# Kernel tuning notes

Measured on AMD Instinct MI355X. Metric: run time of the kernel, lower is better.

The kernel has to match this reference:

```python
import jax, jax.numpy as jnp
import numpy as np

WIN = 4          # ka_win_num (2x2 grid of windows)
KS = 3           # kernel_size
HEADS = 8
PAD = 1


def setup_inputs() -> dict:
    key = jax.random.key(0)
    ks = jax.random.split(key, 11)
    B, res, C = 8, 256, 64
    c16 = C // 16  # SE bottleneck (dim >= 64 branch)
    inp = {
        "x": jax.random.normal(ks[0], (B, res * res, C), dtype=jnp.float32),
        # per-window grouped-conv weights (the "kernels" fed to attention)
        "conv_w": jax.random.normal(ks[1], (WIN, C, C, KS, KS), dtype=jnp.float32) * 0.05,
        "qkv_w": jax.random.normal(ks[2], (C, 3 * C), dtype=jnp.float32) * 0.05,
        "qkv_b": jax.random.normal(ks[3], (3 * C,), dtype=jnp.float32) * 0.01,
        "proj_w": jax.random.normal(ks[4], (C, C), dtype=jnp.float32) * 0.05,
        "proj_b": jax.random.normal(ks[5], (C,), dtype=jnp.float32) * 0.01,
        # per-window SE params (1x1 convs on pooled (k,k))
        "se_w1": jax.random.normal(ks[6], (WIN, c16, C), dtype=jnp.float32) * 0.1,
        "se_b1": jax.random.normal(ks[7], (WIN, c16), dtype=jnp.float32) * 0.01,
        "se_w2": jax.random.normal(ks[8], (WIN, C, c16), dtype=jnp.float32) * 0.1,
        "se_b2": jax.random.normal(ks[9], (WIN, C), dtype=jnp.float32) * 0.01,
    }
    return inp


def reference(x, conv_w, qkv_w, qkv_b, proj_w, proj_b, se_w1, se_b1, se_w2, se_b2):
    B, L, C = x.shape
    H = int(round(np.sqrt(L)))
    g = int(round(np.sqrt(WIN)))      # windows per side = 2
    ws = H // g                       # window_size
    hd = C // HEADS
    scale = hd ** (-0.5)
    S = WIN * KS * KS                 # attention sequence length

    xw = x.reshape(B, g, ws, g, ws, C).transpose(1, 3, 0, 5, 2, 4)
    xw = xw.reshape(WIN, B, C, ws, ws)

    # ---- gather conv kernels as tokens: weight.view(out,in,k2).permute(0,2,1), concat over windows
    kern_tok = conv_w.reshape(WIN, C, C, KS * KS).transpose(1, 0, 3, 2).reshape(C, S, C)

    # ---- self-attention over kernel tokens (batch = C_out = dim)
    qkv = kern_tok @ qkv_w + qkv_b                                    # (C, S, 3C)
    qkv = qkv.reshape(C, S, 3, HEADS, hd).transpose(2, 0, 3, 1, 4)     # (3, C, H, S, hd)
    q, kk, v = qkv[0] * scale, qkv[1], qkv[2]
    attn = jax.nn.softmax(jnp.einsum('chsd,chtd->chst', q, kk), axis=-1)
    out = jnp.einsum('chst,chtd->chsd', attn, v)                       # (C, H, S, hd)
    out = out.transpose(0, 2, 1, 3).reshape(C, S, C)
    out = out @ proj_w + proj_b

    kern = out.reshape(C, WIN, KS, KS, C).transpose(1, 0, 4, 2, 3)

    # ---- SE over each window's kernel, treating (C_out, C_in, k, k) as (N, Ch, H, W)
    pool = kern.mean(axis=(-2, -1))
    h = jax.nn.relu(jnp.einsum('wnc,wdc->wnd', pool, se_w1) + se_b1[:, None, :])
    s = jax.nn.sigmoid(jnp.einsum('wnd,wcd->wnc', h, se_w2) + se_b2[:, None, :])
    kern = kern * s[..., None, None]

    def conv(xi, wi):
        return jax.lax.conv_general_dilated(xi, wi, (1, 1), [(PAD, PAD), (PAD, PAD)])

    y = jax.vmap(conv)(xw, kern)

    y = y.reshape(g, g, B, C, ws, ws).transpose(2, 0, 4, 1, 5, 3).reshape(B, H * H, C)
    return y
```

## Files before the change

kernel.cpp:

```cpp
#include <hip/hip_runtime.h>
#include <hip/hip_bf16.h>

typedef __bf16 bf16x8 __attribute__((ext_vector_type(8)));
typedef float  f32x4  __attribute__((ext_vector_type(4)));

__global__ __launch_bounds__(192) void qkv_kernel(
    const float* __restrict__ conv_w, const float* __restrict__ qkv_w,
    const float* __restrict__ qkv_b,
    float* __restrict__ qv, float* __restrict__ kvv, float* __restrict__ vv)
{
    __shared__ float tok[64];
    const int bid = blockIdx.x;
    const int co = bid / 36, s = bid - co * 36;
    const int w = s / 9, p = s - w * 9;
    const int t = threadIdx.x;
    if (t < 64) tok[t] = conv_w[(((w * 64 + co) * 64 + t) * 9) + p];
    __syncthreads();
    float acc = qkv_b[t];
#pragma unroll 8
    for (int ci = 0; ci < 64; ++ci) acc += tok[ci] * qkv_w[ci * 192 + t];
    const int trip = t >> 6, rem = t & 63, h = rem >> 3, d = rem & 7;
    if (trip == 0) acc *= 0.35355339059327373f;
    float* dst = (trip == 0) ? qv : ((trip == 1) ? kvv : vv);
    dst[((co * 8 + h) * 36 + s) * 8 + d] = acc;
}

__global__ __launch_bounds__(64) void attn_kernel(
    const float* __restrict__ qv, const float* __restrict__ kvv,
    const float* __restrict__ vv, float* __restrict__ ao)
{
    __shared__ float kl[288], vl[288];
    const int bid = blockIdx.x;
    const int t = threadIdx.x;
    const float* kb = kvv + bid * 288;
    const float* vb = vv + bid * 288;
    for (int i = t; i < 288; i += 64) { kl[i] = kb[i]; vl[i] = vb[i]; }
    __syncthreads();
    if (t < 36) {
        float q[8];
        const float* qb = qv + bid * 288 + t * 8;
#pragma unroll
        for (int d = 0; d < 8; ++d) q[d] = qb[d];
        float sc[36];
        float mx = -1e30f;
#pragma unroll
        for (int u = 0; u < 36; ++u) {
            float a = 0.f;
#pragma unroll
            for (int d = 0; d < 8; ++d) a += q[d] * kl[u * 8 + d];
            sc[u] = a;
            mx = fmaxf(mx, a);
        }
        float sum = 0.f;
        float o[8] = {0.f,0.f,0.f,0.f,0.f,0.f,0.f,0.f};
#pragma unroll
        for (int u = 0; u < 36; ++u) {
            float e = expf(sc[u] - mx);
            sum += e;
#pragma unroll
            for (int d = 0; d < 8; ++d) o[d] += e * vl[u * 8 + d];
        }
        const float inv = 1.0f / sum;
        const int co = bid >> 3, h = bid & 7;
        float* dst = ao + (co * 36 + t) * 64 + h * 8;
#pragma unroll
        for (int d = 0; d < 8; ++d) dst[d] = o[d] * inv;
    }
}

__global__ __launch_bounds__(64) void proj_se_kernel(
    const float* __restrict__ ao, const float* __restrict__ proj_w,
    const float* __restrict__ proj_b,
    const float* __restrict__ se_w1, const float* __restrict__ se_b1,
    const float* __restrict__ se_w2, const float* __restrict__ se_b2,
    ushort* __restrict__ kout)
{
    __shared__ float al[9][64];
    __shared__ float pool[64];
    __shared__ float hb[4];
    const int bid = blockIdx.x;
    const int w = bid >> 6, co = bid & 63;
    const int t = threadIdx.x;
    for (int i = t; i < 576; i += 64) {
        int p = i >> 6, j = i & 63;
        al[p][j] = ao[(co * 36 + w * 9 + p) * 64 + j];
    }
    __syncthreads();
    float kv[9];
#pragma unroll
    for (int p = 0; p < 9; ++p) {
        float a = proj_b[t];
#pragma unroll 8
        for (int j = 0; j < 64; ++j) a += al[p][j] * proj_w[j * 64 + t];
        kv[p] = a;
    }
    float pl = 0.f;
#pragma unroll
    for (int p = 0; p < 9; ++p) pl += kv[p];
    pool[t] = pl * (1.0f / 9.0f);
    __syncthreads();
    if (t < 4) {
        float hh = se_b1[w * 4 + t];
#pragma unroll 8
        for (int c = 0; c < 64; ++c) hh += pool[c] * se_w1[(w * 4 + t) * 64 + c];
        hb[t] = fmaxf(hh, 0.0f);
    }
    __syncthreads();
    float z = se_b2[w * 64 + t];
#pragma unroll
    for (int d = 0; d < 4; ++d) z += hb[d] * se_w2[(w * 64 + t) * 4 + d];
    const float sg = 1.0f / (1.0f + expf(-z));
    const int hhalf = t >> 5, ci32 = t & 31;
#pragma unroll
    for (int p = 0; p < 9; ++p) {
        __hip_bfloat16 hv = __float2bfloat16(kv[p] * sg);
        kout[(((hhalf * 4 + w) * 9) + p) * 2048 + co * 32 + ci32] = *(const ushort*)&hv;
    }
}

__global__ __launch_bounds__(256, 3) void conv_kernel(
    const float* __restrict__ x, const ushort* __restrict__ kern,
    float* __restrict__ out)
{
    __shared__ alignas(16) ushort in_lds[18 * 18 * 64];
    __shared__ alignas(16) ushort kn_lds[2 * 2048];

    const int tid = threadIdx.x;

    const int bid = blockIdx.x;
    const int nb  = ((bid & 7) << 8) + (bid >> 3);
    const int bz  = nb >> 6;
    const int rem = nb & 63;
    const int i0  = (rem >> 3) << 4;
    const int j0  = (rem & 7) << 4;
    const int w = bz >> 3, b = bz & 7;
    const int gi = w >> 1, gj = w & 1;

    const int wv   = tid >> 6;
    const int lane = tid & 63;
    const int l15  = lane & 15;
    const int hi4  = lane >> 4;

    const char* kern_b = (const char*)kern;
    const int ksrc = (lane << 4) ^ (((lane >> 3) & 3) << 4);
    auto stage_kern = [&](int s, int buf) {
        const int p = s >> 1, hh = s & 1;
        const char* gs = kern_b + ((size_t)((((hh * 4 + w) * 9)) + p) << 12);
        __builtin_amdgcn_global_load_lds(
            (const __attribute__((address_space(1))) unsigned int*)(gs + (wv << 10) + ksrc),
            (__attribute__((address_space(3))) unsigned int*)
                ((char*)kn_lds + (buf << 12) + (wv << 10)),
            16, 0, 0);
    };

    {
        const int cc = (tid & 15) << 2;
        const int p0 = tid >> 4;
#pragma unroll
        for (int half = 0; half < 2; ++half) {
            const int kbeg = half ? 11 : 0;
            const int kend = half ? 21 : 11;
            float4 v[11];
            unsigned okm = 0;
#pragma unroll
            for (int k = kbeg; k < kend; ++k) {
                const int pp = p0 + (k << 4);
                const int ppc = pp < 323 ? pp : 323;
                const int r = ppc / 18, q = ppc - r * 18;
                const int iy = i0 - 1 + r, jx = j0 - 1 + q;
                const bool ok = (pp < 324) & (iy >= 0) & (iy < 128) & (jx >= 0) & (jx < 128);
                const int iyc = iy < 0 ? 0 : (iy > 127 ? 127 : iy);
                const int jxc = jx < 0 ? 0 : (jx > 127 ? 127 : jx);
                const size_t xi = (((size_t)b << 16) +
                                   (size_t)(gi * 128 + iyc) * 256 + (size_t)(gj * 128 + jxc)) * 64 + cc;
                v[k - kbeg] = *(const float4*)(x + xi);
                okm |= (unsigned)ok << (k - kbeg);
            }
            if (half == 0) stage_kern(0, 0);
#pragma unroll
            for (int k = kbeg; k < kend; ++k) {
                const int pp = p0 + (k << 4);
                if (pp < 324) {
                    const int r = pp / 18, q = pp - r * 18;
                    float4 z = (okm >> (k - kbeg)) & 1 ? v[k - kbeg]
                                                       : make_float4(0.f, 0.f, 0.f, 0.f);
                    union { ushort4 u; ushort h4[4]; } tmp;
                    __hip_bfloat16 b0 = __float2bfloat16(z.x); tmp.h4[0] = *(const ushort*)&b0;
                    __hip_bfloat16 b1 = __float2bfloat16(z.y); tmp.h4[1] = *(const ushort*)&b1;
                    __hip_bfloat16 b2 = __float2bfloat16(z.z); tmp.h4[2] = *(const ushort*)&b2;
                    __hip_bfloat16 b3 = __float2bfloat16(z.w); tmp.h4[3] = *(const ushort*)&b3;
                    *(ushort4*)((char*)in_lds +
                        ((pp << 7) + ((cc << 1) ^ ((q & 7) << 4)))) = tmp.u;
                }
            }
        }
    }

    f32x4 acc[4][4];
#pragma unroll
    for (int mf = 0; mf < 4; ++mf)
#pragma unroll
        for (int nf = 0; nf < 4; ++nf)
            acc[mf][nf] = (f32x4){0.f, 0.f, 0.f, 0.f};

    __syncthreads();

#pragma unroll
    for (int s = 0; s < 18; ++s) {
        const int buf = s & 1;
        if (s < 17) stage_kern(s + 1, buf ^ 1);

        const int p = s >> 1, hh = s & 1;
        const int kh = p / 3, kw = p - kh * 3;

        bf16x8 Kf[4];
#pragma unroll
        for (int nf = 0; nf < 4; ++nf) {
            const int co = nf * 16 + l15;
            Kf[nf] = *(const bf16x8*)((const char*)kn_lds +
                      ((buf << 12) + (co << 6) +
                       ((hi4 << 4) ^ (((co >> 1) & 3) << 4))));
        }

        const int q = l15 + kw;
        const int swz = (q & 7) << 4;
        const int c2 = (hh << 6) | (hi4 << 4);
#pragma unroll
        for (int mf = 0; mf < 4; ++mf) {
            const int r = wv * 4 + mf + kh;
            bf16x8 Af = *(const bf16x8*)((const char*)in_lds +
                          (((r * 18 + q) << 7) + (c2 ^ swz)));
#pragma unroll
            for (int nf = 0; nf < 4; ++nf)
                acc[mf][nf] = __builtin_amdgcn_mfma_f32_16x16x32_bf16(
                    Kf[nf], Af, acc[mf][nf], 0, 0, 0);
        }
        __syncthreads();
    }

    char* ep = (char*)in_lds + (wv << 12);
#pragma unroll
    for (int mf = 0; mf < 4; ++mf) {
        const int iloc = wv * 4 + mf;
        const size_t rowoff = ((size_t)b << 16) +
                              (size_t)(gi * 128 + i0 + iloc) * 256 + (size_t)(gj * 128 + j0);
#pragma unroll
        for (int nf = 0; nf < 4; ++nf) {
            const int off = (nf * 64 + hi4 * 16) ^ ((l15 & 7) << 4);
            *(f32x4*)(ep + l15 * 256 + off) = acc[mf][nf];
        }
#pragma unroll
        for (int t = 0; t < 4; ++t) {
            const int px = t * 4 + hi4;
            f32x4 vv4 = *(const f32x4*)(ep + px * 256 + ((l15 << 4) ^ ((px & 7) << 4)));
            *(f32x4*)(out + (rowoff + px) * 64 + l15 * 4) = vv4;
        }
    }
}

extern "C" void kernel_launch(void* const* d_in, const int* in_sizes, int n_in,
                              void* d_out, int out_size, void* d_ws, size_t ws_size,
                              hipStream_t stream)
{
    const float* x      = (const float*)d_in[0];
    const float* conv_w = (const float*)d_in[1];
    const float* qkv_w  = (const float*)d_in[2];
    const float* qkv_b  = (const float*)d_in[3];
    const float* proj_w = (const float*)d_in[4];
    const float* proj_b = (const float*)d_in[5];
    const float* se_w1  = (const float*)d_in[6];
    const float* se_b1  = (const float*)d_in[7];
    const float* se_w2  = (const float*)d_in[8];
    const float* se_b2  = (const float*)d_in[9];
    float* out = (float*)d_out;

    float* qv = (float*)d_ws;
    float* kv = qv + 147456;
    float* vv = kv + 147456;
    float* ao = vv + 147456;
    ushort* kb = (ushort*)(ao + 147456);

    hipLaunchKernelGGL(qkv_kernel, dim3(2304), dim3(192), 0, stream,
                       conv_w, qkv_w, qkv_b, qv, kv, vv);
    hipLaunchKernelGGL(attn_kernel, dim3(512), dim3(64), 0, stream, qv, kv, vv, ao);
    hipLaunchKernelGGL(proj_se_kernel, dim3(256), dim3(64), 0, stream,
                       ao, proj_w, proj_b, se_w1, se_b1, se_w2, se_b2, kb);
    hipLaunchKernelGGL(conv_kernel, dim3(2048), dim3(256), 0, stream, x, kb, out);
}
```

Measured before the change: 94.42 us.

## Split conv input staging by channel halves and deepen kernel prefetch pipeline

Reorders the conv reduction so that all 9 taps of the first 32 input channels run before the second half. Only half the input tile (32 channels) sits in LDS at a time, which frees LDS and lets launch bounds target 4 blocks per CU instead of 3. The kernel-weight staging becomes a 4-buffer ring prefetched three steps ahead, gated by explicit vmcnt waits and raw barriers. The cost is a mid-loop restage of the input with extra barriers, plus reliance on hand-tuned waitcnt counts.

```diff
diff --git a/kernel.cpp b/kernel.cpp
--- a/kernel.cpp
+++ b/kernel.cpp
@@ -118,12 +118,12 @@
     }
 }
 
-__global__ __launch_bounds__(256, 3) void conv_kernel(
+__global__ __launch_bounds__(256, 4) void conv_kernel(
     const float* __restrict__ x, const ushort* __restrict__ kern,
     float* __restrict__ out)
 {
-    __shared__ alignas(16) ushort in_lds[18 * 18 * 64];
-    __shared__ alignas(16) ushort kn_lds[2 * 2048];
+    __shared__ alignas(16) ushort in_lds[18 * 18 * 32];
+    __shared__ alignas(16) ushort kn_lds[4 * 2048];
 
     const int tid = threadIdx.x;
 
@@ -144,7 +144,8 @@
     const char* kern_b = (const char*)kern;
     const int ksrc = (lane << 4) ^ (((lane >> 3) & 3) << 4);
     auto stage_kern = [&](int s, int buf) {
-        const int p = s >> 1, hh = s & 1;
+        const int hh = (s < 9) ? 0 : 1;
+        const int p  = (s < 9) ? s : s - 9;
         const char* gs = kern_b + ((size_t)((((hh * 4 + w) * 9)) + p) << 12);
         __builtin_amdgcn_global_load_lds(
             (const __attribute__((address_space(1))) unsigned int*)(gs + (wv << 10) + ksrc),
@@ -153,18 +154,18 @@
             16, 0, 0);
     };
 
-    {
-        const int cc = (tid & 15) << 2;
-        const int p0 = tid >> 4;
+    auto stage_input = [&](int h) {
+        const int cc = (tid & 7) << 2;
+        const int p0 = tid >> 3;
 #pragma unroll
         for (int half = 0; half < 2; ++half) {
-            const int kbeg = half ? 11 : 0;
-            const int kend = half ? 21 : 11;
-            float4 v[11];
+            const int kbeg = half ? 6 : 0;
+            const int kend = half ? 11 : 6;
+            float4 v[6];
             unsigned okm = 0;
 #pragma unroll
             for (int k = kbeg; k < kend; ++k) {
-                const int pp = p0 + (k << 4);
+                const int pp = p0 + (k << 5);
                 const int ppc = pp < 323 ? pp : 323;
                 const int r = ppc / 18, q = ppc - r * 18;
                 const int iy = i0 - 1 + r, jx = j0 - 1 + q;
@@ -172,16 +173,15 @@
                 const int iyc = iy < 0 ? 0 : (iy > 127 ? 127 : iy);
                 const int jxc = jx < 0 ? 0 : (jx > 127 ? 127 : jx);
                 const size_t xi = (((size_t)b << 16) +
-                                   (size_t)(gi * 128 + iyc) * 256 + (size_t)(gj * 128 + jxc)) * 64 + cc;
+                                   (size_t)(gi * 128 + iyc) * 256 + (size_t)(gj * 128 + jxc)) * 64 +
+                                  h * 32 + cc;
                 v[k - kbeg] = *(const float4*)(x + xi);
                 okm |= (unsigned)ok << (k - kbeg);
             }
-            if (half == 0) stage_kern(0, 0);
 #pragma unroll
             for (int k = kbeg; k < kend; ++k) {
-                const int pp = p0 + (k << 4);
+                const int pp = p0 + (k << 5);
                 if (pp < 324) {
-                    const int r = pp / 18, q = pp - r * 18;
                     float4 z = (okm >> (k - kbeg)) & 1 ? v[k - kbeg]
                                                        : make_float4(0.f, 0.f, 0.f, 0.f);
                     union { ushort4 u; ushort h4[4]; } tmp;
@@ -190,11 +190,11 @@
                     __hip_bfloat16 b2 = __float2bfloat16(z.z); tmp.h4[2] = *(const ushort*)&b2;
                     __hip_bfloat16 b3 = __float2bfloat16(z.w); tmp.h4[3] = *(const ushort*)&b3;
                     *(ushort4*)((char*)in_lds +
-                        ((pp << 7) + ((cc << 1) ^ ((q & 7) << 4)))) = tmp.u;
+                        ((pp << 6) + ((cc << 1) ^ (((pp >> 1) & 3) << 4)))) = tmp.u;
                 }
             }
         }
-    }
+    };
 
     f32x4 acc[4][4];
 #pragma unroll
@@ -203,14 +203,31 @@
         for (int nf = 0; nf < 4; ++nf)
             acc[mf][nf] = (f32x4){0.f, 0.f, 0.f, 0.f};
 
+    stage_kern(0, 0);
+    stage_kern(1, 1);
+    stage_kern(2, 2);
+    stage_input(0);
     __syncthreads();
 
 #pragma unroll
     for (int s = 0; s < 18; ++s) {
-        const int buf = s & 1;
-        if (s < 17) stage_kern(s + 1, buf ^ 1);
-
-        const int p = s >> 1, hh = s & 1;
+        if (s == 9) {
+            __syncthreads();
+            stage_input(1);
+            __syncthreads();
+        }
+
+        if (s < 16)       asm volatile("s_waitcnt vmcnt(2)" ::: "memory");
+        else if (s == 16) asm volatile("s_waitcnt vmcnt(1)" ::: "memory");
+        else              asm volatile("s_waitcnt vmcnt(0)" ::: "memory");
+        __builtin_amdgcn_sched_barrier(0);
+        __builtin_amdgcn_s_barrier();
+        __builtin_amdgcn_sched_barrier(0);
+
+        if (s <= 14) stage_kern(s + 3, (s + 3) & 3);
+
+        const int buf = s & 3;
+        const int p  = (s < 9) ? s : s - 9;
         const int kh = p / 3, kw = p - kh * 3;
 
         bf16x8 Kf[4];
@@ -223,20 +240,20 @@
         }
 
         const int q = l15 + kw;
-        const int swz = (q & 7) << 4;
-        const int c2 = (hh << 6) | (hi4 << 4);
 #pragma unroll
         for (int mf = 0; mf < 4; ++mf) {
             const int r = wv * 4 + mf + kh;
+            const int px = r * 18 + q;
             bf16x8 Af = *(const bf16x8*)((const char*)in_lds +
-                          (((r * 18 + q) << 7) + (c2 ^ swz)));
+                          ((px << 6) + ((hi4 << 4) ^ (((px >> 1) & 3) << 4))));
 #pragma unroll
             for (int nf = 0; nf < 4; ++nf)
                 acc[mf][nf] = __builtin_amdgcn_mfma_f32_16x16x32_bf16(
                     Kf[nf], Af, acc[mf][nf], 0, 0, 0);
         }
-        __syncthreads();
-    }
+    }
+
+    __syncthreads();
 
     char* ep = (char*)in_lds + (wv << 12);
 #pragma unroll
@@ -255,6 +272,7 @@
             f32x4 vv4 = *(const f32x4*)(ep + px * 256 + ((l15 << 4) ^ ((px & 7) << 4)));
             *(f32x4*)(out + (rowoff + px) * 64 + l15 * 4) = vv4;
         }
+        __builtin_amdgcn_s_barrier();
     }
 }
 
```

Measured after the change: 130.5 us. 38.2% more time.
